# Kernel optimization log

Measured on AMD Instinct MI355X. Metric: run time of the kernel, lower is better.

The kernel has to match this reference:

```python
import jax, jax.numpy as jnp
import numpy as np

B, S, D = 128, 50, 128
NUM_NODE = 40000
SAMPLE = 12
HOP = 2
ALPHA = 0.2  # leaky-relu slope (opt.alpha)


def _leaky(x, slope=ALPHA):
    return jnp.where(x >= 0, x, slope * x)


def setup_inputs() -> dict:
    key = jax.random.key(0)
    ks = jax.random.split(key, 12)
    stdv = 1.0 / float(np.sqrt(D))
    inputs = jax.random.randint(ks[0], (B, S), 0, NUM_NODE)
    adj = jax.random.randint(ks[1], (B, S, S), 0, 5)
    mask_item = jax.random.randint(ks[2], (B, S), 0, 2).at[:, 0].set(1)
    item = jax.random.randint(ks[3], (B, S), 0, NUM_NODE)
    adj_all = jax.random.randint(ks[4], (NUM_NODE, SAMPLE), 0, NUM_NODE)
    num_weight = jax.random.uniform(ks[5], (NUM_NODE, SAMPLE), dtype=jnp.float32)
    embedding = jax.random.uniform(ks[6], (NUM_NODE, D), minval=-stdv, maxval=stdv, dtype=jnp.float32)
    a_local = jax.random.uniform(ks[7], (4, D), minval=-stdv, maxval=stdv, dtype=jnp.float32)
    agg_w1 = jax.random.uniform(ks[8], (HOP, D + 1, D), minval=-stdv, maxval=stdv, dtype=jnp.float32)
    agg_w2 = jax.random.uniform(ks[9], (HOP, D, 1), minval=-stdv, maxval=stdv, dtype=jnp.float32)
    agg_w3 = jax.random.uniform(ks[10], (HOP, 2 * D, D), minval=-stdv, maxval=stdv, dtype=jnp.float32)
    return dict(inputs=inputs, adj=adj, mask_item=mask_item, item=item,
                adj_all=adj_all, num_weight=num_weight, embedding=embedding,
                a_local=a_local, agg_w1=agg_w1, agg_w2=agg_w2, agg_w3=agg_w3)


def _local_agg(h, adj, a_local):
    # e_k[b,i,j] = leakyrelu(sum_d h[b,i,d]*h[b,j,d]*a_k[d]); never materialize [B,N,N,D]
    e = _leaky(jnp.einsum('bid,bjd,kd->kbij', h, h, a_local))  # [4,B,S,S]
    alpha = jnp.full(e.shape[1:], -9e15, dtype=h.dtype)
    for k in range(4):
        alpha = jnp.where(adj == k + 1, e[k], alpha)
    alpha = jax.nn.softmax(alpha, axis=-1)
    return alpha @ h


def _global_agg(w1, w2, w3, self_v, neigh_v, neigh_w, extra):
    # self_v [B,L,D]; neigh_v [B,L,SAMPLE,D]; neigh_w [B,L,SAMPLE]; extra [B,L,D]
    feat = jnp.concatenate([extra[:, :, None, :] * neigh_v, neigh_w[..., None]], axis=-1)  # [B,L,SAMPLE,D+1]
    a = _leaky(feat @ w1, 0.2)                              # [B,L,SAMPLE,D]
    a = jax.nn.softmax((a @ w2)[..., 0], axis=-1)[..., None]  # [B,L,SAMPLE,1]
    neigh = jnp.sum(a * neigh_v, axis=-2)                   # [B,L,D]
    out = jnp.concatenate([self_v, neigh], axis=-1) @ w3    # [B,L,D]
    return jax.nn.relu(out)


def _forward(inputs, adj, mask_item, item, adj_all, num_weight, embedding,
             a_local, agg_w1, agg_w2, agg_w3):
    h = embedding[inputs]                          # [B,S,D]
    h_local = _local_agg(h, adj, a_local)
    # multi-hop neighbor sampling (index_select into adj_all / num)
    item_neighbors = [inputs]
    weight_neighbors = []
    support = S
    for _ in range(HOP):
        last = item_neighbors[-1].reshape(-1)
        support *= SAMPLE
        item_neighbors.append(adj_all[last].reshape(B, support))
        weight_neighbors.append(num_weight[last].reshape(B, support))
    entity = [embedding[idx] for idx in item_neighbors]
    mask_f = mask_item.astype(h.dtype)
    item_emb = embedding[item] * mask_f[..., None]
    session = (jnp.sum(item_emb, 1) / jnp.sum(mask_f, -1, keepdims=True))[:, None, :]  # [B,1,D]
    for n_hop in range(HOP):
        nxt = []
        for hop in range(HOP - n_hop):
            self_v = entity[hop]
            L = self_v.shape[1]
            neigh_v = entity[hop + 1].reshape(B, L, SAMPLE, D)
            neigh_w = weight_neighbors[hop].reshape(B, L, SAMPLE)
            extra = jnp.broadcast_to(session, (B, L, D))
            nxt.append(_global_agg(agg_w1[n_hop], agg_w2[n_hop], agg_w3[n_hop],
                                   self_v, neigh_v, neigh_w, extra))
        entity = nxt
    h_global = entity[0].reshape(B, S, D)
    # dropout_local / dropout_global are identity in eval mode
    return h_local + h_global


def reference(inputs, adj, mask_item, item, adj_all, num_weight, embedding,
              a_local, agg_w1, agg_w2, agg_w3):
    return _forward(inputs, adj, mask_item, item, adj_all, num_weight, embedding,
                    a_local, agg_w1, agg_w2, agg_w3)
```

## Files before the change

### kernel.cpp

```cpp
#include <hip/hip_runtime.h>
#include <math.h>

#define BATCH 128
#define S 50
#define D 128
#define SAMPLE 12

typedef __attribute__((ext_vector_type(8))) short short8v;
typedef __attribute__((ext_vector_type(4))) float f32x4;
typedef unsigned short u16;

__device__ __forceinline__ float leakyf(float x) { return x >= 0.f ? x : 0.2f * x; }
__device__ __forceinline__ u16 f2bf(float f) {
    union { float f; unsigned u; } v; v.f = f;
    unsigned u = v.u;
    return (u16)((u + 0x7FFFu + ((u >> 16) & 1u)) >> 16);
}
__device__ __forceinline__ float bf2f(u16 h) {
    union { float f; unsigned u; } v; v.u = ((unsigned)h) << 16; return v.f;
}

__global__ __launch_bounds__(256) void setup1_kernel(
    const int* __restrict__ item, const int* __restrict__ mask,
    const int* __restrict__ inputs, const int* __restrict__ adj_all,
    const float* __restrict__ num_weight, const float* __restrict__ emb,
    float* __restrict__ session, int* __restrict__ n1, float* __restrict__ nw0)
{
    const int bx = blockIdx.x, t = threadIdx.x;
    if (bx < BATCH) {
        if (t < 128) {
            float num = 0.f, den = 0.f;
            for (int s = 0; s < S; ++s) {
                float m = (float)mask[bx * S + s];
                num += m * emb[item[bx * S + s] * D + t];
                den += m;
            }
            session[bx * D + t] = num / den;
        }
    } else {
        int idx = (bx - BATCH) * 256 + t;
        if (idx < BATCH * 600) {
            int b = idx / 600, j = idx % 600;
            int node = inputs[b * S + j / SAMPLE];
            n1[idx]  = adj_all[node * SAMPLE + j % SAMPLE];
            nw0[idx] = num_weight[node * SAMPLE + j % SAMPLE];
        }
    }
}

__global__ __launch_bounds__(256) void prep2_kernel(
    const float* __restrict__ emb, const float* __restrict__ w1,
    const float* __restrict__ w3, const float* __restrict__ session,
    const int* __restrict__ adj_all, const float* __restrict__ num_weight,
    const int* __restrict__ n1,
    u16* __restrict__ emb_bf, u16* __restrict__ sw1, u16* __restrict__ w3t,
    int* __restrict__ n2, float* __restrict__ nw1)
{
    const int bx = blockIdx.x, t = threadIdx.x;
    if (bx < 2500) {
        int idx = bx * 256 + t;
        const float4* src = reinterpret_cast<const float4*>(emb) + (size_t)idx * 2;
        float4 a = src[0], c = src[1];
        u16 o[8] = {f2bf(a.x), f2bf(a.y), f2bf(a.z), f2bf(a.w),
                    f2bf(c.x), f2bf(c.y), f2bf(c.z), f2bf(c.w)};
        *reinterpret_cast<uint4*>(emb_bf + (size_t)idx * 8) = *reinterpret_cast<uint4*>(o);
    } else if (bx < 2756) {
        int id = bx - 2500, hop = id >> 7, b = id & 127;
        const float* w1s = w1 + hop * 129 * 128;
        const float* se = session + b * 128;
        int n = t >> 1, kh = (t & 1) * 64;
        u16* dst = sw1 + (((size_t)(hop * 128 + b) * 128 + n) * 128) + kh;
        for (int kq = 0; kq < 64; kq += 8) {
            u16 o[8];
            #pragma unroll
            for (int e = 0; e < 8; ++e) { int k = kh + kq + e; o[e] = f2bf(w1s[k * 128 + n] * se[k]); }
            *reinterpret_cast<uint4*>(dst + kq) = *reinterpret_cast<uint4*>(o);
        }
    } else if (bx < 2788) {
        int j = (bx - 2756) * 256 + t;
        int hop = j >> 12, r = j & 4095, n = r >> 5, k0 = (r & 31) * 8;
        const float* w3s = w3 + hop * 256 * 128;
        u16 o[8];
        #pragma unroll
        for (int e = 0; e < 8; ++e) o[e] = f2bf(w3s[(k0 + e) * 128 + n]);
        *reinterpret_cast<uint4*>(w3t + ((size_t)hop * 128 + n) * 256 + k0) = *reinterpret_cast<uint4*>(o);
    } else {
        int idx = (bx - 2788) * 256 + t;
        if (idx < BATCH * 7200) {
            int b = idx / 7200, j = idx % 7200;
            int node = n1[b * 600 + j / SAMPLE];
            n2[idx]  = adj_all[node * SAMPLE + j % SAMPLE];
            nw1[idx] = num_weight[node * SAMPLE + j % SAMPLE];
        }
    }
}

template <int PATH>
__global__ __launch_bounds__(256, 4) void main_kernel(
    const int* __restrict__ inputs, const int* __restrict__ adj,
    const float* __restrict__ emb, const float* __restrict__ a_local,
    const int* __restrict__ n1, const int* __restrict__ n2,
    const float* __restrict__ nw0, const float* __restrict__ nw1,
    const u16* __restrict__ emb_bf, const u16* __restrict__ sw1,
    const float* __restrict__ w1, const float* __restrict__ w2,
    const u16* __restrict__ w3t,
    const u16* __restrict__ in0, const u16* __restrict__ in1,
    u16* __restrict__ o0, u16* __restrict__ o1, float* __restrict__ outf)
{
    __shared__ __align__(16) char smem[37664];
    const int b = blockIdx.y;
    const int t = threadIdx.x;
    const int bx = blockIdx.x;

    if (PATH == 0 && bx == 82) {
        float (*h)[D]     = (float(*)[D])smem;
        float (*al)[D]    = (float(*)[D])(smem + 25600);
        float (*alpha)[S] = (float(*)[S])(smem + 27648);

        for (int idx = t; idx < S * D; idx += 256) {
            int i = idx / D, d = idx % D;
            h[i][d] = emb[inputs[b * S + i] * D + d];
        }
        for (int idx = t; idx < 4 * D; idx += 256) al[idx / D][idx % D] = a_local[idx];
        __syncthreads();

        for (int p = t; p < S * S; p += 256) {
            int i = p / S, j = p % S;
            int a = adj[b * S * S + p];
            float v = -9e15f;
            if (a >= 1 && a <= 4) {
                const float* ak = al[a - 1];
                float dot = 0.f;
                #pragma unroll 4
                for (int d = 0; d < D; ++d) dot += h[i][d] * h[j][d] * ak[d];
                v = leakyf(dot);
            }
            alpha[i][j] = v;
        }
        __syncthreads();

        if (t < S) {
            float m = -INFINITY;
            for (int j = 0; j < S; ++j) m = fmaxf(m, alpha[t][j]);
            float ssum = 0.f;
            for (int j = 0; j < S; ++j) { float e = expf(alpha[t][j] - m); alpha[t][j] = e; ssum += e; }
            float inv = 1.f / ssum;
            for (int j = 0; j < S; ++j) alpha[t][j] *= inv;
        }
        __syncthreads();

        for (int idx = t; idx < S * D; idx += 256) {
            int i = idx / D, d = idx % D;
            float acc = 0.f;
            #pragma unroll 5
            for (int j = 0; j < S; ++j) acc += alpha[i][j] * h[j][d];
            outf[b * S * D + idx] = acc;
        }
        return;
    }

    int mode, l0, L, Lm, hop;
    const u16 *nsrc, *ssrc;
    const int* idxTab; const float* nwTab;
    u16* outb;
    if (PATH == 2)    { mode = 2; l0 = bx * 8;        L = 50;  Lm = 600;  nsrc = in1;    ssrc = in0;    idxTab = nullptr; nwTab = nw0; outb = nullptr; hop = 1; }
    else if (bx < 75) { mode = 1; l0 = bx * 8;        L = 600; Lm = 7200; nsrc = emb_bf; ssrc = emb_bf; idxTab = n2;      nwTab = nw1; outb = o1;      hop = 0; }
    else              { mode = 0; l0 = (bx - 75) * 8; L = 50;  Lm = 600;  nsrc = emb_bf; ssrc = emb_bf; idxTab = n1;      nwTab = nw0; outb = o0;      hop = 0; }

    u16* nvL   = (u16*)smem;
    u16* selfL = (u16*)(smem + 24576);
    float (*score_w)[96] = (float(*)[96])(smem + 28672);
    float* score = (float*)(smem + 30208);
    float* nwgtL = (float*)(smem + 30592);

    const u16*   sw1b   = sw1 + (size_t)(hop * 128 + b) * 16384;
    const float* w1last = w1 + hop * 129 * 128 + 128 * 128;
    const float* w2h    = w2 + hop * 128;
    const u16*   w3th   = w3t + hop * 32768;

    const int lane = t & 63, wv = t >> 6, cn = lane & 15, cg = lane >> 4;
    const int nc0 = (2 * wv) * 16 + cn, nc1 = (2 * wv + 1) * 16 + cn;

    #pragma unroll
    for (int i = 0; i < 6; ++i) {
        int slot = i * 256 + t;
        int mt = slot >> 8, kk = (slot >> 6) & 3;
        int ln2 = slot & 63, cg2 = ln2 >> 4, cn2 = ln2 & 15;
        int gm = l0 * 12 + (cn2 >> 2) * 24 + mt * 4 + (cn2 & 3);
        int gmc = (gm < Lm) ? gm : 0;
        int row = (PATH == 2) ? (b * 600 + gmc) : idxTab[b * Lm + gmc];
        int chunk = kk * 4 + cg2;
        uint4 v = *reinterpret_cast<const uint4*>(nsrc + (size_t)row * 128 + chunk * 8);
        *reinterpret_cast<uint4*>(nvL + slot * 8) = v;
    }
    {
        int kk = t >> 6, ln2 = t & 63, cg2 = ln2 >> 4, i2 = ln2 & 15;
        int l = 2 * (i2 >> 2) + ((i2 >> 1) & 1);
        int lg = l0 + l; if (lg >= L) lg = 0;
        int srow;
        if (PATH == 2) srow = b * 50 + lg;
        else           srow = (mode == 1) ? n1[b * 600 + lg] : inputs[b * S + lg];
        uint4 v = *reinterpret_cast<const uint4*>(ssrc + (size_t)srow * 128 + (kk * 4 + cg2) * 8);
        *reinterpret_cast<uint4*>(selfL + t * 8) = v;
    }
    if (t < 96) {
        int gm = l0 * 12 + t;
        nwgtL[t] = (gm < Lm) ? nwTab[b * Lm + gm] : 0.f;
    }
    __syncthreads();

    f32x4 acc[6][2];
    #pragma unroll
    for (int mt = 0; mt < 6; ++mt) {
        acc[mt][0] = (f32x4){0.f, 0.f, 0.f, 0.f};
        acc[mt][1] = (f32x4){0.f, 0.f, 0.f, 0.f};
    }
    #pragma unroll
    for (int kk = 0; kk < 4; ++kk) {
        int kb = kk * 32 + cg * 8;
        short8v b0 = *reinterpret_cast<const short8v*>(sw1b + nc0 * 128 + kb);
        short8v b1 = *reinterpret_cast<const short8v*>(sw1b + nc1 * 128 + kb);
        #pragma unroll
        for (int mt = 0; mt < 6; ++mt) {
            short8v a = *reinterpret_cast<const short8v*>(nvL + ((mt * 4 + kk) * 64 + lane) * 8);
            acc[mt][0] = __builtin_amdgcn_mfma_f32_16x16x32_bf16(a, b0, acc[mt][0], 0, 0, 0);
            acc[mt][1] = __builtin_amdgcn_mfma_f32_16x16x32_bf16(a, b1, acc[mt][1], 0, 0, 0);
        }
    }

    {
        float w2v0 = w2h[nc0], w2v1 = w2h[nc1];
        float w1l0 = w1last[nc0], w1l1 = w1last[nc1];
        #pragma unroll
        for (int mt = 0; mt < 6; ++mt) {
            #pragma unroll
            for (int r = 0; r < 4; ++r) {
                int m = cg * 24 + mt * 4 + r;
                float nw = nwgtL[m];
                float v = leakyf(acc[mt][0][r] + nw * w1l0) * w2v0 +
                          leakyf(acc[mt][1][r] + nw * w1l1) * w2v1;
                v += __shfl_xor(v, 1); v += __shfl_xor(v, 2);
                v += __shfl_xor(v, 4); v += __shfl_xor(v, 8);
                if (cn == 0) score_w[wv][m] = v;
            }
        }
    }
    __syncthreads();

    if (t < 8) {
        float e[SAMPLE]; float mx = -INFINITY;
        #pragma unroll
        for (int s2 = 0; s2 < SAMPLE; ++s2) {
            int m = t * SAMPLE + s2;
            float v = score_w[0][m] + score_w[1][m] + score_w[2][m] + score_w[3][m];
            e[s2] = v; mx = fmaxf(mx, v);
        }
        float ssum = 0.f;
        #pragma unroll
        for (int s2 = 0; s2 < SAMPLE; ++s2) { e[s2] = expf(e[s2] - mx); ssum += e[s2]; }
        float inv = 1.f / ssum;
        #pragma unroll
        for (int s2 = 0; s2 < SAMPLE; ++s2) score[t * SAMPLE + s2] = e[s2] * inv;
    }
    __syncthreads();

    f32x4 accS0 = (f32x4){0.f, 0.f, 0.f, 0.f};
    f32x4 accS1 = (f32x4){0.f, 0.f, 0.f, 0.f};
    #pragma unroll
    for (int mt = 0; mt < 6; ++mt) {
        acc[mt][0] = (f32x4){0.f, 0.f, 0.f, 0.f};
        acc[mt][1] = (f32x4){0.f, 0.f, 0.f, 0.f};
    }
    #pragma unroll
    for (int kk = 0; kk < 4; ++kk) {
        int kb = kk * 32 + cg * 8;
        short8v by0 = *reinterpret_cast<const short8v*>(w3th + nc0 * 256 + 128 + kb);
        short8v by1 = *reinterpret_cast<const short8v*>(w3th + nc1 * 256 + 128 + kb);
        short8v bs0 = *reinterpret_cast<const short8v*>(w3th + nc0 * 256 + kb);
        short8v bs1 = *reinterpret_cast<const short8v*>(w3th + nc1 * 256 + kb);
        short8v aS = *reinterpret_cast<const short8v*>(selfL + (kk * 64 + lane) * 8);
        accS0 = __builtin_amdgcn_mfma_f32_16x16x32_bf16(aS, bs0, accS0, 0, 0, 0);
        accS1 = __builtin_amdgcn_mfma_f32_16x16x32_bf16(aS, bs1, accS1, 0, 0, 0);
        #pragma unroll
        for (int mt = 0; mt < 6; ++mt) {
            short8v a = *reinterpret_cast<const short8v*>(nvL + ((mt * 4 + kk) * 64 + lane) * 8);
            acc[mt][0] = __builtin_amdgcn_mfma_f32_16x16x32_bf16(a, by0, acc[mt][0], 0, 0, 0);
            acc[mt][1] = __builtin_amdgcn_mfma_f32_16x16x32_bf16(a, by1, acc[mt][1], 0, 0, 0);
        }
    }
    float P00 = 0.f, P01 = 0.f, P10 = 0.f, P11 = 0.f;
    #pragma unroll
    for (int mt = 0; mt < 6; ++mt) {
        #pragma unroll
        for (int r = 0; r < 4; ++r) {
            float al = score[cg * 24 + mt * 4 + r];
            if (mt < 3) { P00 += al * acc[mt][0][r]; P01 += al * acc[mt][1][r]; }
            else        { P10 += al * acc[mt][0][r]; P11 += al * acc[mt][1][r]; }
        }
    }
    {
        float v00 = fmaxf(P00 + accS0[0], 0.f);
        float v01 = fmaxf(P01 + accS1[0], 0.f);
        float v10 = fmaxf(P10 + accS0[2], 0.f);
        float v11 = fmaxf(P11 + accS1[2], 0.f);
        int lg0 = l0 + cg * 2, lg1 = lg0 + 1;
        if (PATH == 2) {
            if (lg0 < L) {
                float* p = outf + ((size_t)b * 50 + lg0) * 128;
                p[nc0] += v00; p[nc1] += v01;
            }
            if (lg1 < L) {
                float* p = outf + ((size_t)b * 50 + lg1) * 128;
                p[nc0] += v10; p[nc1] += v11;
            }
        } else {
            if (lg0 < L) {
                u16* p = outb + ((size_t)b * L + lg0) * 128;
                p[nc0] = f2bf(v00); p[nc1] = f2bf(v01);
            }
            if (lg1 < L) {
                u16* p = outb + ((size_t)b * L + lg1) * 128;
                p[nc0] = f2bf(v10); p[nc1] = f2bf(v11);
            }
        }
    }
}

extern "C" void kernel_launch(void* const* d_in, const int* in_sizes, int n_in,
                              void* d_out, int out_size, void* d_ws, size_t ws_size,
                              hipStream_t stream)
{
    const int*   inputs     = (const int*)d_in[0];
    const int*   adj        = (const int*)d_in[1];
    const int*   mask_item  = (const int*)d_in[2];
    const int*   item       = (const int*)d_in[3];
    const int*   adj_all    = (const int*)d_in[4];
    const float* num_weight = (const float*)d_in[5];
    const float* embedding  = (const float*)d_in[6];
    const float* a_local    = (const float*)d_in[7];
    const float* agg_w1     = (const float*)d_in[8];
    const float* agg_w2     = (const float*)d_in[9];
    const float* agg_w3     = (const float*)d_in[10];
    float* out = (float*)d_out;

    char* w = (char*)d_ws;
    float* ws_session = (float*)(w);
    int*   ws_n1      = (int*)(w + 65536);
    float* ws_nw0     = (float*)(w + 372736);
    int*   ws_n2      = (int*)(w + 679936);
    float* ws_nw1     = (float*)(w + 4366336);
    u16*   ws_emb     = (u16*)(w + 8052736);
    u16*   ws_sw1     = (u16*)(w + 18292736);
    u16*   ws_w3t     = (u16*)(w + 26681344);
    u16*   ws_out0    = (u16*)(w + 26812416);
    u16*   ws_out1    = (u16*)(w + 28450816);

    setup1_kernel<<<dim3(BATCH + 300), 256, 0, stream>>>(
        item, mask_item, inputs, adj_all, num_weight, embedding,
        ws_session, ws_n1, ws_nw0);
    prep2_kernel<<<dim3(6388), 256, 0, stream>>>(
        embedding, agg_w1, agg_w3, ws_session, adj_all, num_weight, ws_n1,
        ws_emb, ws_sw1, ws_w3t, ws_n2, ws_nw1);

    main_kernel<0><<<dim3(83, BATCH), 256, 0, stream>>>(
        inputs, adj, embedding, a_local, ws_n1, ws_n2, ws_nw0, ws_nw1,
        ws_emb, ws_sw1, agg_w1, agg_w2, ws_w3t,
        nullptr, nullptr, ws_out0, ws_out1, out);

    main_kernel<2><<<dim3(7, BATCH), 256, 0, stream>>>(
        inputs, adj, embedding, a_local, ws_n1, ws_n2, ws_nw0, ws_nw1,
        ws_emb, ws_sw1, agg_w1, agg_w2, ws_w3t,
        ws_out0, ws_out1, nullptr, nullptr, out);
}
```

Measured before the change: 332.0 us.

## Pre-permute gather offsets, shrink LDS and registers, bf16 local-agg block

Prep now writes the hop-2 and hop-1 neighbor index tables already permuted into the MFMA tile order and pre-shifted to byte offsets, so the main kernel's gather drops its index arithmetic and the dependent index lookup. The main kernel splits the second MFMA stage into two sequential column passes and computes the per-lane softmax in registers from a transposed score buffer. This removes the separate softmax sync stage and halves the accumulator registers, which together with the smaller shared buffer allows raising the occupancy target to 5 blocks per CU. The local-attention block moves to block 0 and reads bf16 embeddings through a transposed, padded shared layout, using fast exp. Risks are reduced precision in the local branch and spills under the tighter register budget.

```diff
diff --git a/kernel.cpp b/kernel.cpp
--- a/kernel.cpp
+++ b/kernel.cpp
@@ -54,7 +54,7 @@
     const int* __restrict__ adj_all, const float* __restrict__ num_weight,
     const int* __restrict__ n1,
     u16* __restrict__ emb_bf, u16* __restrict__ sw1, u16* __restrict__ w3t,
-    int* __restrict__ n2, float* __restrict__ nw1)
+    int* __restrict__ n2p, int* __restrict__ n1p, float* __restrict__ nw1)
 {
     const int bx = blockIdx.x, t = threadIdx.x;
     if (bx < 2500) {
@@ -84,44 +84,58 @@
         #pragma unroll
         for (int e = 0; e < 8; ++e) o[e] = f2bf(w3s[(k0 + e) * 128 + n]);
         *reinterpret_cast<uint4*>(w3t + ((size_t)hop * 128 + n) * 256 + k0) = *reinterpret_cast<uint4*>(o);
-    } else {
+    } else if (bx < 6388) {
         int idx = (bx - 2788) * 256 + t;
         if (idx < BATCH * 7200) {
-            int b = idx / 7200, j = idx % 7200;
-            int node = n1[b * 600 + j / SAMPLE];
-            n2[idx]  = adj_all[node * SAMPLE + j % SAMPLE];
-            nw1[idx] = num_weight[node * SAMPLE + j % SAMPLE];
+            int b = idx / 7200, r = idx % 7200;
+            int lblk = r / 96, q = r % 96;
+            int i = q >> 4, c = q & 15;
+            int gm = lblk * 96 + (c >> 2) * 24 + i * 4 + (c & 3);
+            int node = n1[b * 600 + gm / SAMPLE];
+            int s = gm % SAMPLE;
+            n2p[idx] = adj_all[node * SAMPLE + s] << 8;
+            nw1[b * 7200 + gm] = num_weight[node * SAMPLE + s];
+        }
+    } else {
+        int idx = (bx - 6388) * 256 + t;
+        if (idx < BATCH * 672) {
+            int b = idx / 672, r = idx % 672;
+            int lblk = r / 96, q = r % 96;
+            int i = q >> 4, c = q & 15;
+            int gm = lblk * 96 + (c >> 2) * 24 + i * 4 + (c & 3);
+            int jc = (gm < 600) ? gm : 0;
+            n1p[idx] = n1[b * 600 + jc] << 8;
         }
     }
 }
 
 template <int PATH>
-__global__ __launch_bounds__(256, 4) void main_kernel(
+__global__ __launch_bounds__(256, 5) void main_kernel(
     const int* __restrict__ inputs, const int* __restrict__ adj,
-    const float* __restrict__ emb, const float* __restrict__ a_local,
-    const int* __restrict__ n1, const int* __restrict__ n2,
+    const u16* __restrict__ emb_bf, const float* __restrict__ a_local,
+    const int* __restrict__ n1, const int* __restrict__ n2p,
+    const int* __restrict__ n1p,
     const float* __restrict__ nw0, const float* __restrict__ nw1,
-    const u16* __restrict__ emb_bf, const u16* __restrict__ sw1,
-    const float* __restrict__ w1, const float* __restrict__ w2,
-    const u16* __restrict__ w3t,
+    const u16* __restrict__ sw1, const float* __restrict__ w1,
+    const float* __restrict__ w2, const u16* __restrict__ w3t,
     const u16* __restrict__ in0, const u16* __restrict__ in1,
     u16* __restrict__ o0, u16* __restrict__ o1, float* __restrict__ outf)
 {
-    __shared__ __align__(16) char smem[37664];
+    __shared__ __align__(16) char smem[30592];
     const int b = blockIdx.y;
     const int t = threadIdx.x;
     const int bx = blockIdx.x;
 
-    if (PATH == 0 && bx == 82) {
-        float (*h)[D]     = (float(*)[D])smem;
-        float (*al)[D]    = (float(*)[D])(smem + 25600);
-        float (*alpha)[S] = (float(*)[S])(smem + 27648);
+    if (PATH == 0 && bx == 0) {
+        u16*   ht    = (u16*)smem;
+        float* alpha = (float*)(smem + 13312);
+        u16*   alb   = (u16*)(smem + 23520);
 
         for (int idx = t; idx < S * D; idx += 256) {
-            int i = idx / D, d = idx % D;
-            h[i][d] = emb[inputs[b * S + i] * D + d];
-        }
-        for (int idx = t; idx < 4 * D; idx += 256) al[idx / D][idx % D] = a_local[idx];
+            int i = idx >> 7, d = idx & 127;
+            ht[d * 52 + i] = emb_bf[(size_t)inputs[b * S + i] * D + d];
+        }
+        for (int idx = t; idx < 512; idx += 256) alb[idx] = f2bf(a_local[idx]);
         __syncthreads();
 
         for (int p = t; p < S * S; p += 256) {
@@ -129,49 +143,50 @@
             int a = adj[b * S * S + p];
             float v = -9e15f;
             if (a >= 1 && a <= 4) {
-                const float* ak = al[a - 1];
+                const u16* ak = alb + (a - 1) * D;
                 float dot = 0.f;
                 #pragma unroll 4
-                for (int d = 0; d < D; ++d) dot += h[i][d] * h[j][d] * ak[d];
+                for (int d = 0; d < D; ++d)
+                    dot += bf2f(ht[d * 52 + i]) * bf2f(ht[d * 52 + j]) * bf2f(ak[d]);
                 v = leakyf(dot);
             }
-            alpha[i][j] = v;
+            alpha[i * 51 + j] = v;
         }
         __syncthreads();
 
         if (t < S) {
             float m = -INFINITY;
-            for (int j = 0; j < S; ++j) m = fmaxf(m, alpha[t][j]);
+            for (int j = 0; j < S; ++j) m = fmaxf(m, alpha[t * 51 + j]);
             float ssum = 0.f;
-            for (int j = 0; j < S; ++j) { float e = expf(alpha[t][j] - m); alpha[t][j] = e; ssum += e; }
+            for (int j = 0; j < S; ++j) { float e = __expf(alpha[t * 51 + j] - m); alpha[t * 51 + j] = e; ssum += e; }
             float inv = 1.f / ssum;
-            for (int j = 0; j < S; ++j) alpha[t][j] *= inv;
+            for (int j = 0; j < S; ++j) alpha[t * 51 + j] *= inv;
         }
         __syncthreads();
 
         for (int idx = t; idx < S * D; idx += 256) {
-            int i = idx / D, d = idx % D;
+            int i = idx >> 7, d = idx & 127;
             float acc = 0.f;
             #pragma unroll 5
-            for (int j = 0; j < S; ++j) acc += alpha[i][j] * h[j][d];
-            outf[b * S * D + idx] = acc;
+            for (int j = 0; j < S; ++j) acc += alpha[i * 51 + j] * bf2f(ht[d * 52 + j]);
+            outf[(size_t)b * S * D + idx] = acc;
         }
         return;
     }
 
-    int mode, l0, L, Lm, hop;
+    int mode, lblk, L, Lm, hop;
     const u16 *nsrc, *ssrc;
-    const int* idxTab; const float* nwTab;
+    const int* ptab; const float* nwTab;
     u16* outb;
-    if (PATH == 2)    { mode = 2; l0 = bx * 8;        L = 50;  Lm = 600;  nsrc = in1;    ssrc = in0;    idxTab = nullptr; nwTab = nw0; outb = nullptr; hop = 1; }
-    else if (bx < 75) { mode = 1; l0 = bx * 8;        L = 600; Lm = 7200; nsrc = emb_bf; ssrc = emb_bf; idxTab = n2;      nwTab = nw1; outb = o1;      hop = 0; }
-    else              { mode = 0; l0 = (bx - 75) * 8; L = 50;  Lm = 600;  nsrc = emb_bf; ssrc = emb_bf; idxTab = n1;      nwTab = nw0; outb = o0;      hop = 0; }
-
-    u16* nvL   = (u16*)smem;
-    u16* selfL = (u16*)(smem + 24576);
-    float (*score_w)[96] = (float(*)[96])(smem + 28672);
-    float* score = (float*)(smem + 30208);
-    float* nwgtL = (float*)(smem + 30592);
+    if (PATH == 2)    { mode = 2; lblk = bx;     L = 50;  Lm = 600;  hop = 1; nsrc = in1;    ssrc = in0;    ptab = nullptr;                   nwTab = nw0; outb = nullptr; }
+    else if (bx >= 8) { mode = 1; lblk = bx - 8; L = 600; Lm = 7200; hop = 0; nsrc = emb_bf; ssrc = emb_bf; ptab = n2p + (b * 75 + lblk) * 96; nwTab = nw1; outb = o1; }
+    else              { mode = 0; lblk = bx - 1; L = 50;  Lm = 600;  hop = 0; nsrc = emb_bf; ssrc = emb_bf; ptab = n1p + (b * 7 + lblk) * 96;  nwTab = nw0; outb = o0; }
+    const int l0 = lblk * 8;
+
+    u16*   nvL     = (u16*)smem;
+    u16*   selfL   = (u16*)(smem + 24576);
+    float* score_w = (float*)(smem + 28672);
+    float* nwgtL   = (float*)(smem + 30208);
 
     const u16*   sw1b   = sw1 + (size_t)(hop * 128 + b) * 16384;
     const float* w1last = w1 + hop * 129 * 128 + 128 * 128;
@@ -180,27 +195,30 @@
 
     const int lane = t & 63, wv = t >> 6, cn = lane & 15, cg = lane >> 4;
     const int nc0 = (2 * wv) * 16 + cn, nc1 = (2 * wv + 1) * 16 + cn;
+    const int c = t & 15;
+    const int chunk = t >> 4;
 
     #pragma unroll
     for (int i = 0; i < 6; ++i) {
-        int slot = i * 256 + t;
-        int mt = slot >> 8, kk = (slot >> 6) & 3;
-        int ln2 = slot & 63, cg2 = ln2 >> 4, cn2 = ln2 & 15;
-        int gm = l0 * 12 + (cn2 >> 2) * 24 + mt * 4 + (cn2 & 3);
-        int gmc = (gm < Lm) ? gm : 0;
-        int row = (PATH == 2) ? (b * 600 + gmc) : idxTab[b * Lm + gmc];
-        int chunk = kk * 4 + cg2;
-        uint4 v = *reinterpret_cast<const uint4*>(nsrc + (size_t)row * 128 + chunk * 8);
-        *reinterpret_cast<uint4*>(nvL + slot * 8) = v;
+        int off;
+        if (PATH == 2) {
+            int gm = l0 * 12 + (c >> 2) * 24 + i * 4 + (c & 3);
+            if (gm > 599) gm = 599;
+            off = (b * 600 + gm) << 8;
+        } else {
+            off = ptab[i * 16 + c];
+        }
+        uint4 v = *reinterpret_cast<const uint4*>((const char*)nsrc + (unsigned)off + chunk * 16);
+        *reinterpret_cast<uint4*>(nvL + (i * 256 + t) * 8) = v;
     }
     {
-        int kk = t >> 6, ln2 = t & 63, cg2 = ln2 >> 4, i2 = ln2 & 15;
-        int l = 2 * (i2 >> 2) + ((i2 >> 1) & 1);
+        int l = 2 * (c >> 2) + ((c >> 1) & 1);
         int lg = l0 + l; if (lg >= L) lg = 0;
         int srow;
-        if (PATH == 2) srow = b * 50 + lg;
-        else           srow = (mode == 1) ? n1[b * 600 + lg] : inputs[b * S + lg];
-        uint4 v = *reinterpret_cast<const uint4*>(ssrc + (size_t)srow * 128 + (kk * 4 + cg2) * 8);
+        if (PATH == 2)      srow = b * 50 + lg;
+        else if (mode == 1) srow = n1[b * 600 + lg];
+        else                srow = inputs[b * S + lg];
+        uint4 v = *reinterpret_cast<const uint4*>(ssrc + (size_t)srow * 128 + chunk * 8);
         *reinterpret_cast<uint4*>(selfL + t * 8) = v;
     }
     if (t < 96) {
@@ -227,7 +245,6 @@
             acc[mt][1] = __builtin_amdgcn_mfma_f32_16x16x32_bf16(a, b1, acc[mt][1], 0, 0, 0);
         }
     }
-
     {
         float w2v0 = w2h[nc0], w2v1 = w2h[nc1];
         float w1l0 = w1last[nc0], w1l1 = w1last[nc1];
@@ -241,87 +258,68 @@
                           leakyf(acc[mt][1][r] + nw * w1l1) * w2v1;
                 v += __shfl_xor(v, 1); v += __shfl_xor(v, 2);
                 v += __shfl_xor(v, 4); v += __shfl_xor(v, 8);
-                if (cn == 0) score_w[wv][m] = v;
+                if (cn == 0) score_w[m * 4 + wv] = v;
             }
         }
     }
     __syncthreads();
 
-    if (t < 8) {
-        float e[SAMPLE]; float mx = -INFINITY;
-        #pragma unroll
-        for (int s2 = 0; s2 < SAMPLE; ++s2) {
-            int m = t * SAMPLE + s2;
-            float v = score_w[0][m] + score_w[1][m] + score_w[2][m] + score_w[3][m];
-            e[s2] = v; mx = fmaxf(mx, v);
-        }
-        float ssum = 0.f;
-        #pragma unroll
-        for (int s2 = 0; s2 < SAMPLE; ++s2) { e[s2] = expf(e[s2] - mx); ssum += e[s2]; }
-        float inv = 1.f / ssum;
-        #pragma unroll
-        for (int s2 = 0; s2 < SAMPLE; ++s2) score[t * SAMPLE + s2] = e[s2] * inv;
-    }
-    __syncthreads();
-
-    f32x4 accS0 = (f32x4){0.f, 0.f, 0.f, 0.f};
-    f32x4 accS1 = (f32x4){0.f, 0.f, 0.f, 0.f};
+    float alph[24];
+    {
+        const f32x4* sw4 = reinterpret_cast<const f32x4*>(score_w);
+        float mx0 = -1e30f, mx1 = -1e30f;
+        #pragma unroll
+        for (int q = 0; q < 24; ++q) {
+            f32x4 s4 = sw4[cg * 24 + q];
+            float s = (s4[0] + s4[1]) + (s4[2] + s4[3]);
+            alph[q] = s;
+            if (q < 12) mx0 = fmaxf(mx0, s); else mx1 = fmaxf(mx1, s);
+        }
+        float sm0 = 0.f, sm1 = 0.f;
+        #pragma unroll
+        for (int q = 0; q < 12; ++q) { alph[q] = __expf(alph[q] - mx0); sm0 += alph[q]; }
+        #pragma unroll
+        for (int q = 12; q < 24; ++q) { alph[q] = __expf(alph[q] - mx1); sm1 += alph[q]; }
+        float i0 = 1.f / sm0, i1 = 1.f / sm1;
+        #pragma unroll
+        for (int q = 0; q < 12; ++q) alph[q] *= i0;
+        #pragma unroll
+        for (int q = 12; q < 24; ++q) alph[q] *= i1;
+    }
+
     #pragma unroll
-    for (int mt = 0; mt < 6; ++mt) {
-        acc[mt][0] = (f32x4){0.f, 0.f, 0.f, 0.f};
-        acc[mt][1] = (f32x4){0.f, 0.f, 0.f, 0.f};
-    }
-    #pragma unroll
-    for (int kk = 0; kk < 4; ++kk) {
-        int kb = kk * 32 + cg * 8;
-        short8v by0 = *reinterpret_cast<const short8v*>(w3th + nc0 * 256 + 128 + kb);
-        short8v by1 = *reinterpret_cast<const short8v*>(w3th + nc1 * 256 + 128 + kb);
-        short8v bs0 = *reinterpret_cast<const short8v*>(w3th + nc0 * 256 + kb);
-        short8v bs1 = *reinterpret_cast<const short8v*>(w3th + nc1 * 256 + kb);
-        short8v aS = *reinterpret_cast<const short8v*>(selfL + (kk * 64 + lane) * 8);
-        accS0 = __builtin_amdgcn_mfma_f32_16x16x32_bf16(aS, bs0, accS0, 0, 0, 0);
-        accS1 = __builtin_amdgcn_mfma_f32_16x16x32_bf16(aS, bs1, accS1, 0, 0, 0);
-        #pragma unroll
-        for (int mt = 0; mt < 6; ++mt) {
-            short8v a = *reinterpret_cast<const short8v*>(nvL + ((mt * 4 + kk) * 64 + lane) * 8);
-            acc[mt][0] = __builtin_amdgcn_mfma_f32_16x16x32_bf16(a, by0, acc[mt][0], 0, 0, 0);
-            acc[mt][1] = __builtin_amdgcn_mfma_f32_16x16x32_bf16(a, by1, acc[mt][1], 0, 0, 0);
-        }
-    }
-    float P00 = 0.f, P01 = 0.f, P10 = 0.f, P11 = 0.f;
-    #pragma unroll
-    for (int mt = 0; mt < 6; ++mt) {
-        #pragma unroll
-        for (int r = 0; r < 4; ++r) {
-            float al = score[cg * 24 + mt * 4 + r];
-            if (mt < 3) { P00 += al * acc[mt][0][r]; P01 += al * acc[mt][1][r]; }
-            else        { P10 += al * acc[mt][0][r]; P11 += al * acc[mt][1][r]; }
-        }
-    }
-    {
-        float v00 = fmaxf(P00 + accS0[0], 0.f);
-        float v01 = fmaxf(P01 + accS1[0], 0.f);
-        float v10 = fmaxf(P10 + accS0[2], 0.f);
-        float v11 = fmaxf(P11 + accS1[2], 0.f);
+    for (int j = 0; j < 2; ++j) {
+        int nc = (2 * wv + j) * 16 + cn;
+        f32x4 Y[6]; f32x4 Ys = (f32x4){0.f, 0.f, 0.f, 0.f};
+        #pragma unroll
+        for (int mt = 0; mt < 6; ++mt) Y[mt] = (f32x4){0.f, 0.f, 0.f, 0.f};
+        #pragma unroll
+        for (int kk = 0; kk < 4; ++kk) {
+            int kb = kk * 32 + cg * 8;
+            short8v bw = *reinterpret_cast<const short8v*>(w3th + nc * 256 + 128 + kb);
+            short8v bs = *reinterpret_cast<const short8v*>(w3th + nc * 256 + kb);
+            short8v aS = *reinterpret_cast<const short8v*>(selfL + (kk * 64 + lane) * 8);
+            Ys = __builtin_amdgcn_mfma_f32_16x16x32_bf16(aS, bs, Ys, 0, 0, 0);
+            #pragma unroll
+            for (int mt = 0; mt < 6; ++mt) {
+                short8v a = *reinterpret_cast<const short8v*>(nvL + ((mt * 4 + kk) * 64 + lane) * 8);
+                Y[mt] = __builtin_amdgcn_mfma_f32_16x16x32_bf16(a, bw, Y[mt], 0, 0, 0);
+            }
+        }
+        float P0 = 0.f, P1 = 0.f;
+        #pragma unroll
+        for (int q = 0; q < 12; ++q) P0 += alph[q] * Y[q >> 2][q & 3];
+        #pragma unroll
+        for (int q = 12; q < 24; ++q) P1 += alph[q] * Y[q >> 2][q & 3];
+        float v0 = fmaxf(P0 + Ys[0], 0.f);
+        float v1 = fmaxf(P1 + Ys[2], 0.f);
         int lg0 = l0 + cg * 2, lg1 = lg0 + 1;
         if (PATH == 2) {
-            if (lg0 < L) {
-                float* p = outf + ((size_t)b * 50 + lg0) * 128;
-                p[nc0] += v00; p[nc1] += v01;
-            }
-            if (lg1 < L) {
-                float* p = outf + ((size_t)b * 50 + lg1) * 128;
-                p[nc0] += v10; p[nc1] += v11;
-            }
+            if (lg0 < L) { float* p = outf + ((size_t)b * 50 + lg0) * 128 + nc; *p += v0; }
+            if (lg1 < L) { float* p = outf + ((size_t)b * 50 + lg1) * 128 + nc; *p += v1; }
         } else {
-            if (lg0 < L) {
-                u16* p = outb + ((size_t)b * L + lg0) * 128;
-                p[nc0] = f2bf(v00); p[nc1] = f2bf(v01);
-            }
-            if (lg1 < L) {
-                u16* p = outb + ((size_t)b * L + lg1) * 128;
-                p[nc0] = f2bf(v10); p[nc1] = f2bf(v11);
-            }
+            if (lg0 < L) outb[((size_t)b * L + lg0) * 128 + nc] = f2bf(v0);
+            if (lg1 < L) outb[((size_t)b * L + lg1) * 128 + nc] = f2bf(v1);
         }
     }
 }
@@ -347,28 +345,29 @@
     float* ws_session = (float*)(w);
     int*   ws_n1      = (int*)(w + 65536);
     float* ws_nw0     = (float*)(w + 372736);
-    int*   ws_n2      = (int*)(w + 679936);
-    float* ws_nw1     = (float*)(w + 4366336);
-    u16*   ws_emb     = (u16*)(w + 8052736);
-    u16*   ws_sw1     = (u16*)(w + 18292736);
-    u16*   ws_w3t     = (u16*)(w + 26681344);
-    u16*   ws_out0    = (u16*)(w + 26812416);
-    u16*   ws_out1    = (u16*)(w + 28450816);
+    float* ws_nw1     = (float*)(w + 679936);
+    int*   ws_n2p     = (int*)(w + 4366336);
+    int*   ws_n1p     = (int*)(w + 8052736);
+    u16*   ws_emb     = (u16*)(w + 8396800);
+    u16*   ws_sw1     = (u16*)(w + 18636800);
+    u16*   ws_w3t     = (u16*)(w + 27025408);
+    u16*   ws_out0    = (u16*)(w + 27156480);
+    u16*   ws_out1    = (u16*)(w + 28794880);
 
     setup1_kernel<<<dim3(BATCH + 300), 256, 0, stream>>>(
         item, mask_item, inputs, adj_all, num_weight, embedding,
         ws_session, ws_n1, ws_nw0);
-    prep2_kernel<<<dim3(6388), 256, 0, stream>>>(
+    prep2_kernel<<<dim3(6724), 256, 0, stream>>>(
         embedding, agg_w1, agg_w3, ws_session, adj_all, num_weight, ws_n1,
-        ws_emb, ws_sw1, ws_w3t, ws_n2, ws_nw1);
+        ws_emb, ws_sw1, ws_w3t, ws_n2p, ws_n1p, ws_nw1);
 
     main_kernel<0><<<dim3(83, BATCH), 256, 0, stream>>>(
-        inputs, adj, embedding, a_local, ws_n1, ws_n2, ws_nw0, ws_nw1,
-        ws_emb, ws_sw1, agg_w1, agg_w2, ws_w3t,
+        inputs, adj, ws_emb, a_local, ws_n1, ws_n2p, ws_n1p, ws_nw0, ws_nw1,
+        ws_sw1, agg_w1, agg_w2, ws_w3t,
         nullptr, nullptr, ws_out0, ws_out1, out);
 
     main_kernel<2><<<dim3(7, BATCH), 256, 0, stream>>>(
-        inputs, adj, embedding, a_local, ws_n1, ws_n2, ws_nw0, ws_nw1,
-        ws_emb, ws_sw1, agg_w1, agg_w2, ws_w3t,
+        inputs, adj, ws_emb, a_local, ws_n1, ws_n2p, ws_n1p, ws_nw0, ws_nw1,
+        ws_sw1, agg_w1, agg_w2, ws_w3t,
         ws_out0, ws_out1, nullptr, nullptr, out);
 }
```

After: 530.3 us. 1.6x slower.
